# Kernel tuning notes

Hardware: AMD Instinct MI355X
Metric: run time of the kernel (lower is better)

## Reference

```python
import jax, jax.numpy as jnp
import numpy as np

N_NODES = 50000
N_EDGES = 800000
IN_FEATS = 128
OUT_FEATS = 128


def setup_inputs() -> dict:
    key = jax.random.key(0)
    k_feat, k_src, k_dst, k_w1, k_w2, k_lw = jax.random.split(key, 6)
    feat = jax.random.normal(k_feat, (N_NODES, IN_FEATS), dtype=jnp.float32)
    src_idx = jax.random.randint(k_src, (N_EDGES,), 0, N_NODES, dtype=jnp.int64 if jax.config.jax_enable_x64 else jnp.int32)
    dst_idx = jax.random.randint(k_dst, (N_EDGES,), 0, N_NODES, dtype=jnp.int64 if jax.config.jax_enable_x64 else jnp.int32)
    # xavier-uniform-ish scales
    w1_lim = float(np.sqrt(6.0 / (2 * IN_FEATS + IN_FEATS)))
    w2_lim = float(np.sqrt(6.0 / (IN_FEATS + OUT_FEATS)))
    lw_lim = float(np.sqrt(2.0) * np.sqrt(6.0 / (IN_FEATS + OUT_FEATS)))
    weight1 = jax.random.uniform(k_w1, (2 * IN_FEATS, IN_FEATS), jnp.float32, -w1_lim, w1_lim)
    weight2 = jax.random.uniform(k_w2, (IN_FEATS, OUT_FEATS), jnp.float32, -w2_lim, w2_lim)
    loop_weight = jax.random.uniform(k_lw, (IN_FEATS, OUT_FEATS), jnp.float32, -lw_lim, lw_lim)
    bias = jnp.zeros((OUT_FEATS,), dtype=jnp.float32)
    return {
        "feat": feat,
        "src_idx": src_idx,
        "dst_idx": dst_idx,
        "weight1": weight1,
        "weight2": weight2,
        "loop_weight": loop_weight,
        "bias": bias,
    }


def reference(feat, src_idx, dst_idx, weight1, weight2, loop_weight, bias):
    # Gather per-edge src/dst features and concat: [E, 2*d]
    feat_msg = jnp.concatenate([feat[src_idx], feat[dst_idx]], axis=-1)
    # 2-layer edge MLP: relu(msg @ W1) @ W2 -> [E, out]
    e_msg = jnp.matmul(jax.nn.relu(jnp.matmul(feat_msg, weight1)), weight2)
    # Scatter-sum to destination nodes: [N, out]
    rst = jax.ops.segment_sum(e_msg, dst_idx, num_segments=feat.shape[0])
    # bias + residual loop message
    rst = rst + bias + jnp.matmul(feat, loop_weight)
    return rst
```

## Files before the change

### kernel.cpp

```cpp
#include <hip/hip_runtime.h>

typedef __attribute__((ext_vector_type(8))) unsigned short ushort8v;
typedef __attribute__((ext_vector_type(8))) short short8v;
typedef __attribute__((ext_vector_type(4))) float f32x4;

#define CAP 64
#define BINSTRIDE 2560

__device__ inline unsigned short f2bf(float f) {
    union { float f; unsigned u; } v; v.f = f;
    unsigned u = v.u;
    unsigned r = (u + 0x7FFFu + ((u >> 16) & 1u)) >> 16;
    return (unsigned short)r;
}
__device__ inline float bf2f(unsigned short h) {
    union { unsigned u; float f; } v; v.u = ((unsigned)h) << 16;
    return v.f;
}
__device__ inline unsigned pkbf(float lo, float hi) {
    unsigned r;
    asm("v_cvt_pk_bf16_f32 %0, %1, %2" : "=v"(r) : "v"(lo), "v"(hi));
    return r;
}

__global__ __launch_bounds__(256) void prep_weights(
    const float* __restrict__ W1, const float* __restrict__ W2,
    const float* __restrict__ LW,
    unsigned short* __restrict__ W1t, unsigned short* __restrict__ W3t,
    int* __restrict__ binCur, int NBINS) {
    int tid = threadIdx.x;
    if (blockIdx.x == 0)
        for (int j = tid; j < NBINS; j += 256) binCur[j] = 0;
    int i = blockIdx.x * 256 + tid;
    if (i < 32768) {
        int jj = i >> 7, k = i & 127;
        float v = (jj < 128) ? W1[k * 128 + jj] : W1[(128 + k) * 128 + (jj - 128)];
        W1t[i] = f2bf(v);
    } else {
        int i2 = i - 32768;
        int n = i2 >> 8, k = i2 & 255;
        float v = (k < 128) ? W2[k * 128 + n] : LW[(k - 128) * 128 + n];
        W3t[i2] = f2bf(v);
    }
}

__global__ __launch_bounds__(256) void gemm1_bin(
    const float* __restrict__ feat, const unsigned short* __restrict__ W1t,
    unsigned short* __restrict__ AB,
    const int* __restrict__ src, const int* __restrict__ dst,
    int* __restrict__ binCur, unsigned* __restrict__ binPairs,
    int E, int NC, int NT2, int M, int NBINS) {
    __shared__ unsigned short smem[2 * 128 * 64];
    const int tid = threadIdx.x;
    const int bid = blockIdx.x;
    const int r5 = bid % 5;

    if (r5 < 4) {
        int g = (bid / 5) * 4 + r5;
        if (g >= NT2) return;
        int m0 = (g >> 1) * 128, n0 = (g & 1) * 128;
        const int lane = tid & 63, w = tid >> 6;
        const int wr = w >> 1, wc = w & 1;
        const int q = lane >> 4, ln = lane & 15;
        unsigned short* As = smem;
        unsigned short* Bs = smem + 128 * 64;

        f32x4 acc[4][4];
#pragma unroll
        for (int i = 0; i < 4; i++)
#pragma unroll
            for (int j = 0; j < 4; j++) acc[i][j] = (f32x4)0.f;

        for (int kk = 0; kk < 128; kk += 64) {
#pragma unroll
            for (int i = 0; i < 4; i++) {
                int id = i * 256 + tid;
                int r = id >> 3, bb = id & 7, gr = m0 + r;
                unsigned short* dstp = As + r * 64 + ((bb ^ (r & 7)) * 8);
                float4 lo = make_float4(0.f, 0.f, 0.f, 0.f), hi = lo;
                if (gr < M) {
                    const float* p = feat + (size_t)gr * 128 + kk + bb * 8;
                    lo = *(const float4*)p;
                    hi = *(const float4*)(p + 4);
                }
                *(uint4*)dstp = make_uint4(pkbf(lo.x, lo.y), pkbf(lo.z, lo.w),
                                           pkbf(hi.x, hi.y), pkbf(hi.z, hi.w));
            }
#pragma unroll
            for (int i = 0; i < 4; i++) {
                int id = i * 256 + tid;
                int r = id >> 3, bb = id & 7;
                ushort8v v = *(const ushort8v*)(W1t + (size_t)(n0 + r) * 128 + kk + bb * 8);
                *(ushort8v*)(Bs + r * 64 + ((bb ^ (r & 7)) * 8)) = v;
            }
            __syncthreads();
#pragma unroll
            for (int ks = 0; ks < 2; ks++) {
                short8v af[4], bv[4];
#pragma unroll
                for (int ti = 0; ti < 4; ti++) {
                    int m = wr * 64 + ti * 16 + ln;
                    int blk = (ks * 4 + q) ^ (m & 7);
                    af[ti] = *(const short8v*)(As + m * 64 + blk * 8);
                }
#pragma unroll
                for (int tj = 0; tj < 4; tj++) {
                    int n = wc * 64 + tj * 16 + ln;
                    int blk = (ks * 4 + q) ^ (n & 7);
                    bv[tj] = *(const short8v*)(Bs + n * 64 + blk * 8);
                }
#pragma unroll
                for (int ti = 0; ti < 4; ti++)
#pragma unroll
                    for (int tj = 0; tj < 4; tj++)
                        acc[ti][tj] = __builtin_amdgcn_mfma_f32_16x16x32_bf16(
                            af[ti], bv[tj], acc[ti][tj], 0, 0, 0);
            }
            if (kk == 0) __syncthreads();
        }
#pragma unroll
        for (int ti = 0; ti < 4; ti++) {
            int rowb = m0 + wr * 64 + ti * 16 + q * 4;
#pragma unroll
            for (int tj = 0; tj < 4; tj++) {
                int col = n0 + wc * 64 + tj * 16 + ln;
                f32x4 c = acc[ti][tj];
#pragma unroll
                for (int r = 0; r < 4; r++) {
                    int row = rowb + r;
                    if (row < M)
                        AB[(size_t)row * 256 + col] = f2bf(c[r]);
                }
            }
        }
    } else {
        int chunk = bid / 5;
        if (chunk >= NC) return;
        int* hist = (int*)smem;
        int* bse = hist + 512;
        for (int j = tid; j < NBINS; j += 256) hist[j] = 0;

        int s[16], d[16];
        int base = chunk * 4096;
#pragma unroll
        for (int i = 0; i < 4; i++) {
            int e = base + i * 1024 + tid * 4;
            if (e + 3 < E) {
                int4 dv = *(const int4*)(dst + e);
                int4 sv = *(const int4*)(src + e);
                d[i * 4 + 0] = dv.x; d[i * 4 + 1] = dv.y;
                d[i * 4 + 2] = dv.z; d[i * 4 + 3] = dv.w;
                s[i * 4 + 0] = sv.x; s[i * 4 + 1] = sv.y;
                s[i * 4 + 2] = sv.z; s[i * 4 + 3] = sv.w;
            } else {
#pragma unroll
                for (int k = 0; k < 4; k++) {
                    int ee = e + k;
                    if (ee < E) { d[i * 4 + k] = dst[ee]; s[i * 4 + k] = src[ee]; }
                    else d[i * 4 + k] = -1;
                }
            }
        }
        __syncthreads();
#pragma unroll
        for (int k = 0; k < 16; k++)
            if (d[k] >= 0) atomicAdd(&hist[d[k] >> 7], 1);
        __syncthreads();
        for (int j = tid; j < NBINS; j += 256) {
            int c = hist[j];
            bse[j] = c ? atomicAdd(&binCur[j], c) : 0;
            hist[j] = 0;
        }
        __syncthreads();
#pragma unroll
        for (int k = 0; k < 16; k++) {
            if (d[k] < 0) continue;
            int b = d[k] >> 7;
            int p = bse[b] + atomicAdd(&hist[b], 1);
            if (p < BINSTRIDE)
                binPairs[(size_t)b * BINSTRIDE + p] =
                    ((unsigned)(d[k] & 127) << 16) | (unsigned)s[k];
        }
    }
}

__global__ __launch_bounds__(256) void build_buckets(
    const int* __restrict__ binCur, const unsigned* __restrict__ binPairs,
    int* __restrict__ cur, unsigned short* __restrict__ eSrc,
    int N, int NBINS) {
    __shared__ unsigned pairs[BINSTRIDE];
    __shared__ int deg[128], rnk[128];
    int b = blockIdx.x, tid = threadIdx.x;
    if (b >= NBINS) return;
    int cnt = min(binCur[b], BINSTRIDE);
    if (tid < 128) { deg[tid] = 0; rnk[tid] = 0; }
    __syncthreads();
    for (int i = tid; i < cnt; i += 256) {
        unsigned pr = binPairs[(size_t)b * BINSTRIDE + i];
        pairs[i] = pr;
        atomicAdd(&deg[pr >> 16], 1);
    }
    __syncthreads();
    int node0 = b << 7;
    if (tid < 128 && node0 + tid < N) cur[node0 + tid] = deg[tid];
    for (int i = tid; i < cnt; i += 256) {
        unsigned pr = pairs[i];
        int dl = pr >> 16;
        int pos = atomicAdd(&rnk[dl], 1);
        if (pos < CAP)
            eSrc[(size_t)(node0 + dl) * CAP + pos] = (unsigned short)(pr & 0xFFFF);
    }
}

__global__ __launch_bounds__(256) void gather_kernel(
    const unsigned short* __restrict__ AB, const int* __restrict__ cur,
    const unsigned short* __restrict__ eSrc,
    unsigned short* __restrict__ S2, int N) {
    int wid = (blockIdx.x * 256 + threadIdx.x) >> 6;
    int lane = threadIdx.x & 63;
    if (wid >= N) return;
    int num = min(cur[wid], CAP);
    size_t start = (size_t)wid * CAP;
    int half = lane >> 5, ln32 = lane & 31;
    ushort4 bv = *(const ushort4*)(AB + (size_t)wid * 256 + 128 + ln32 * 4);
    float b0 = bf2f(bv.x), b1 = bf2f(bv.y), b2 = bf2f(bv.z), b3 = bf2f(bv.w);
    float p0 = 0.f, p1 = 0.f, p2 = 0.f, p3 = 0.f;

    int mySrc = (lane < num) ? (int)eSrc[start + lane] : 0;
    int j = 0;
    for (; j + 16 <= num; j += 16) {
        ushort4 v[8];
#pragma unroll
        for (int u = 0; u < 8; u++) {
            int s = __shfl(mySrc, j + 2 * u + half);
            v[u] = *(const ushort4*)(AB + (size_t)s * 256 + ln32 * 4);
        }
#pragma unroll
        for (int u = 0; u < 8; u++) {
            p0 += fmaxf(bf2f(v[u].x) + b0, 0.f);
            p1 += fmaxf(bf2f(v[u].y) + b1, 0.f);
            p2 += fmaxf(bf2f(v[u].z) + b2, 0.f);
            p3 += fmaxf(bf2f(v[u].w) + b3, 0.f);
        }
    }
    for (; j + 4 <= num; j += 4) {
        ushort4 v[2];
#pragma unroll
        for (int u = 0; u < 2; u++) {
            int s = __shfl(mySrc, j + 2 * u + half);
            v[u] = *(const ushort4*)(AB + (size_t)s * 256 + ln32 * 4);
        }
#pragma unroll
        for (int u = 0; u < 2; u++) {
            p0 += fmaxf(bf2f(v[u].x) + b0, 0.f);
            p1 += fmaxf(bf2f(v[u].y) + b1, 0.f);
            p2 += fmaxf(bf2f(v[u].z) + b2, 0.f);
            p3 += fmaxf(bf2f(v[u].w) + b3, 0.f);
        }
    }
    for (; j < num; j += 2) {
        int idx = j + half;
        int s = __shfl(mySrc, idx);
        bool ok = idx < num;
        ushort4 v = *(const ushort4*)(AB + (size_t)s * 256 + ln32 * 4);
        float m = ok ? 1.f : 0.f;
        p0 += m * fmaxf(bf2f(v.x) + b0, 0.f);
        p1 += m * fmaxf(bf2f(v.y) + b1, 0.f);
        p2 += m * fmaxf(bf2f(v.z) + b2, 0.f);
        p3 += m * fmaxf(bf2f(v.w) + b3, 0.f);
    }
    p0 += __shfl_xor(p0, 32);
    p1 += __shfl_xor(p1, 32);
    p2 += __shfl_xor(p2, 32);
    p3 += __shfl_xor(p3, 32);
    if (half == 0) {
        *(ushort4*)(S2 + (size_t)wid * 128 + ln32 * 4) =
            make_ushort4(f2bf(p0), f2bf(p1), f2bf(p2), f2bf(p3));
    }
}

__global__ __launch_bounds__(256) void gemm2_kernel(
    const unsigned short* __restrict__ S2, const float* __restrict__ feat,
    const unsigned short* __restrict__ W3t,
    float* __restrict__ out, const float* __restrict__ bias, int M) {
    __shared__ unsigned short smem[2 * 128 * 64];
    unsigned short* As = smem;
    unsigned short* Bs = smem + 128 * 64;
    const int tid = threadIdx.x;
    const int lane = tid & 63, w = tid >> 6;
    const int wr = w >> 1, wc = w & 1;
    const int q = lane >> 4, ln = lane & 15;
    const int m0 = blockIdx.x * 128;

    f32x4 acc[4][4];
#pragma unroll
    for (int i = 0; i < 4; i++)
#pragma unroll
        for (int j = 0; j < 4; j++) acc[i][j] = (f32x4)0.f;

    for (int kk = 0; kk < 256; kk += 64) {
        const bool aF32 = (kk >= 128);
#pragma unroll
        for (int i = 0; i < 4; i++) {
            int id = i * 256 + tid;
            int r = id >> 3, bb = id & 7, gr = m0 + r;
            unsigned short* dstp = As + r * 64 + ((bb ^ (r & 7)) * 8);
            if (aF32) {
                float4 lo = make_float4(0.f, 0.f, 0.f, 0.f), hi = lo;
                if (gr < M) {
                    const float* p = feat + (size_t)gr * 128 + (kk - 128) + bb * 8;
                    lo = *(const float4*)p;
                    hi = *(const float4*)(p + 4);
                }
                *(uint4*)dstp = make_uint4(pkbf(lo.x, lo.y), pkbf(lo.z, lo.w),
                                           pkbf(hi.x, hi.y), pkbf(hi.z, hi.w));
            } else {
                ushort8v v = (ushort8v)(unsigned short)0;
                if (gr < M) v = *(const ushort8v*)(S2 + (size_t)gr * 128 + kk + bb * 8);
                *(ushort8v*)dstp = v;
            }
        }
#pragma unroll
        for (int i = 0; i < 4; i++) {
            int id = i * 256 + tid;
            int r = id >> 3, bb = id & 7;
            ushort8v v = *(const ushort8v*)(W3t + (size_t)r * 256 + kk + bb * 8);
            *(ushort8v*)(Bs + r * 64 + ((bb ^ (r & 7)) * 8)) = v;
        }
        __syncthreads();
#pragma unroll
        for (int ks = 0; ks < 2; ks++) {
            short8v af[4], bv[4];
#pragma unroll
            for (int ti = 0; ti < 4; ti++) {
                int m = wr * 64 + ti * 16 + ln;
                int blk = (ks * 4 + q) ^ (m & 7);
                af[ti] = *(const short8v*)(As + m * 64 + blk * 8);
            }
#pragma unroll
            for (int tj = 0; tj < 4; tj++) {
                int n = wc * 64 + tj * 16 + ln;
                int blk = (ks * 4 + q) ^ (n & 7);
                bv[tj] = *(const short8v*)(Bs + n * 64 + blk * 8);
            }
#pragma unroll
            for (int ti = 0; ti < 4; ti++)
#pragma unroll
                for (int tj = 0; tj < 4; tj++)
                    acc[ti][tj] = __builtin_amdgcn_mfma_f32_16x16x32_bf16(
                        af[ti], bv[tj], acc[ti][tj], 0, 0, 0);
        }
        if (kk + 64 < 256) __syncthreads();
    }

#pragma unroll
    for (int ti = 0; ti < 4; ti++) {
        int rowb = m0 + wr * 64 + ti * 16 + q * 4;
#pragma unroll
        for (int tj = 0; tj < 4; tj++) {
            int col = wc * 64 + tj * 16 + ln;
            f32x4 c = acc[ti][tj];
            float bv = bias[col];
#pragma unroll
            for (int r = 0; r < 4; r++) {
                int row = rowb + r;
                if (row < M)
                    out[(size_t)row * 128 + col] = c[r] + bv;
            }
        }
    }
}

extern "C" void kernel_launch(void* const* d_in, const int* in_sizes, int n_in,
                              void* d_out, int out_size, void* d_ws, size_t ws_size,
                              hipStream_t stream) {
    const float* feat = (const float*)d_in[0];
    const int* src = (const int*)d_in[1];
    const int* dst = (const int*)d_in[2];
    const float* W1 = (const float*)d_in[3];
    const float* W2 = (const float*)d_in[4];
    const float* LW = (const float*)d_in[5];
    const float* bias = (const float*)d_in[6];
    float* out = (float*)d_out;

    const int N = in_sizes[0] / 128;
    const int E = in_sizes[1];
    const int NBINS = (N + 127) / 128;

    char* ws = (char*)d_ws;
    unsigned short* S2 = (unsigned short*)ws;
    size_t off = (size_t)N * 128 * 2;
    unsigned short* AB = (unsigned short*)(ws + off);
    off += (size_t)N * 256 * 2;
    unsigned short* W1t = (unsigned short*)(ws + off);
    off += (size_t)256 * 128 * 2;
    unsigned short* W3t = (unsigned short*)(ws + off);
    off += (size_t)128 * 256 * 2;
    int* cur = (int*)(ws + off);
    off += (size_t)N * 4;
    unsigned short* eSrc = (unsigned short*)(ws + off);
    off += (size_t)N * CAP * 2;
    int* binCur = (int*)(ws + off);
    off += (size_t)NBINS * 4;
    unsigned* binPairs = (unsigned*)(ws + off);
    off += (size_t)NBINS * BINSTRIDE * 4;

    prep_weights<<<256, 256, 0, stream>>>(W1, W2, LW, W1t, W3t, binCur, NBINS);

    int NT2 = ((N + 127) / 128) * 2;
    int NC = (E + 4095) / 4096;
    int NG = (NT2 + 3) / 4;
    int mx = NG > NC ? NG : NC;
    gemm1_bin<<<5 * mx, 256, 0, stream>>>(
        feat, W1t, AB, src, dst, binCur, binPairs, E, NC, NT2, N, NBINS);

    build_buckets<<<NBINS, 256, 0, stream>>>(binCur, binPairs, cur, eSrc, N, NBINS);

    gather_kernel<<<(N + 3) / 4, 256, 0, stream>>>(AB, cur, eSrc, S2, N);

    gemm2_kernel<<<(N + 127) / 128, 256, 0, stream>>>(S2, feat, W3t, out, bias, N);
}
```

Measured before the change: 164.3 us.

## Restructure pipeline: fuse binning with weight prep, loop GEMM with gemm1 and bucket build

Edge binning moves into the weight-prep kernel, and the bin counter is cleared with a memset. The self-loop GEMM (feat @ LoopW + bias) now runs as a third N-tile inside gemm1 and writes out directly. Bucket building runs in the same launch as gemm1, so one kernel launch and one pass over feat in gemm2 go away. The gather kernel now uses 16-byte loads with four edges per iteration. gemm2 shrinks to K=128 and accumulates into out with a read-modify-write, which adds an extra read of out in exchange for fewer launches and less feat traffic.

```diff
diff --git a/kernel.cpp b/kernel.cpp
--- a/kernel.cpp
+++ b/kernel.cpp
@@ -23,47 +23,103 @@
     return r;
 }
 
-__global__ __launch_bounds__(256) void prep_weights(
+__global__ __launch_bounds__(256) void prep_bin(
     const float* __restrict__ W1, const float* __restrict__ W2,
     const float* __restrict__ LW,
-    unsigned short* __restrict__ W1t, unsigned short* __restrict__ W3t,
-    int* __restrict__ binCur, int NBINS) {
-    int tid = threadIdx.x;
-    if (blockIdx.x == 0)
-        for (int j = tid; j < NBINS; j += 256) binCur[j] = 0;
-    int i = blockIdx.x * 256 + tid;
-    if (i < 32768) {
-        int jj = i >> 7, k = i & 127;
-        float v = (jj < 128) ? W1[k * 128 + jj] : W1[(128 + k) * 128 + (jj - 128)];
-        W1t[i] = f2bf(v);
-    } else {
-        int i2 = i - 32768;
-        int n = i2 >> 8, k = i2 & 255;
-        float v = (k < 128) ? W2[k * 128 + n] : LW[(k - 128) * 128 + n];
-        W3t[i2] = f2bf(v);
-    }
-}
-
-__global__ __launch_bounds__(256) void gemm1_bin(
-    const float* __restrict__ feat, const unsigned short* __restrict__ W1t,
-    unsigned short* __restrict__ AB,
+    unsigned short* __restrict__ W1t, unsigned short* __restrict__ W2t,
+    unsigned short* __restrict__ LWt,
     const int* __restrict__ src, const int* __restrict__ dst,
     int* __restrict__ binCur, unsigned* __restrict__ binPairs,
-    int E, int NC, int NT2, int M, int NBINS) {
+    int E, int NCHUNK, int NBINS) {
+    __shared__ int hist[512];
+    __shared__ int bse[512];
+    const int tid = threadIdx.x;
+    const int bid = blockIdx.x;
+
+    if (bid < 256) {
+        int i = bid * 256 + tid;
+        if (i < 32768) {
+            int n = i >> 7, k = i & 127;
+            float v = (n < 128) ? W1[k * 128 + n] : W1[(128 + k) * 128 + (n - 128)];
+            W1t[i] = f2bf(v);
+        } else if (i < 49152) {
+            int i2 = i - 32768;
+            int n = i2 >> 7, k = i2 & 127;
+            W2t[i2] = f2bf(W2[k * 128 + n]);
+        } else {
+            int i3 = i - 49152;
+            int n = i3 >> 7, k = i3 & 127;
+            LWt[i3] = f2bf(LW[k * 128 + n]);
+        }
+        return;
+    }
+    int chunk = bid - 256;
+    if (chunk >= NCHUNK) return;
+    for (int j = tid; j < NBINS; j += 256) hist[j] = 0;
+
+    int s[8], d[8];
+    int base = chunk * 2048 + tid * 8;
+    if (base + 7 < E) {
+        int4 s0 = *(const int4*)(src + base);
+        int4 s1 = *(const int4*)(src + base + 4);
+        int4 d0 = *(const int4*)(dst + base);
+        int4 d1 = *(const int4*)(dst + base + 4);
+        s[0] = s0.x; s[1] = s0.y; s[2] = s0.z; s[3] = s0.w;
+        s[4] = s1.x; s[5] = s1.y; s[6] = s1.z; s[7] = s1.w;
+        d[0] = d0.x; d[1] = d0.y; d[2] = d0.z; d[3] = d0.w;
+        d[4] = d1.x; d[5] = d1.y; d[6] = d1.z; d[7] = d1.w;
+    } else {
+#pragma unroll
+        for (int k = 0; k < 8; k++) {
+            int ee = base + k;
+            if (ee < E) { d[k] = dst[ee]; s[k] = src[ee]; }
+            else d[k] = -1;
+        }
+    }
+    __syncthreads();
+#pragma unroll
+    for (int k = 0; k < 8; k++)
+        if (d[k] >= 0) atomicAdd(&hist[d[k] >> 7], 1);
+    __syncthreads();
+    for (int j = tid; j < NBINS; j += 256) {
+        int c = hist[j];
+        bse[j] = c ? atomicAdd(&binCur[j], c) : 0;
+        hist[j] = 0;
+    }
+    __syncthreads();
+#pragma unroll
+    for (int k = 0; k < 8; k++) {
+        if (d[k] < 0) continue;
+        int b = d[k] >> 7;
+        int p = bse[b] + atomicAdd(&hist[b], 1);
+        if (p < BINSTRIDE)
+            binPairs[(size_t)b * BINSTRIDE + p] =
+                ((unsigned)(d[k] & 127) << 16) | (unsigned)s[k];
+    }
+}
+
+__global__ __launch_bounds__(256) void gemm1_build(
+    const float* __restrict__ feat, const unsigned short* __restrict__ W1t,
+    const unsigned short* __restrict__ LWt, const float* __restrict__ bias,
+    unsigned short* __restrict__ AB, float* __restrict__ out,
+    const int* __restrict__ binCur, const unsigned* __restrict__ binPairs,
+    int* __restrict__ cur, unsigned short* __restrict__ eSrc,
+    int M, int NBINS) {
     __shared__ unsigned short smem[2 * 128 * 64];
     const int tid = threadIdx.x;
     const int bid = blockIdx.x;
-    const int r5 = bid % 5;
-
-    if (r5 < 4) {
-        int g = (bid / 5) * 4 + r5;
-        if (g >= NT2) return;
-        int m0 = (g >> 1) * 128, n0 = (g & 1) * 128;
+    const int r4 = bid & 3;
+
+    if (r4 < 3) {
+        const int m0 = (bid >> 2) * 128;
+        const int nt = r4;
         const int lane = tid & 63, w = tid >> 6;
         const int wr = w >> 1, wc = w & 1;
         const int q = lane >> 4, ln = lane & 15;
         unsigned short* As = smem;
         unsigned short* Bs = smem + 128 * 64;
+        const unsigned short* Bsrc = (nt < 2) ? (W1t + (size_t)(nt * 128) * 128)
+                                              : LWt;
 
         f32x4 acc[4][4];
 #pragma unroll
@@ -90,7 +146,7 @@
             for (int i = 0; i < 4; i++) {
                 int id = i * 256 + tid;
                 int r = id >> 3, bb = id & 7;
-                ushort8v v = *(const ushort8v*)(W1t + (size_t)(n0 + r) * 128 + kk + bb * 8);
+                ushort8v v = *(const ushort8v*)(Bsrc + (size_t)r * 128 + kk + bb * 8);
                 *(ushort8v*)(Bs + r * 64 + ((bb ^ (r & 7)) * 8)) = v;
             }
             __syncthreads();
@@ -123,92 +179,45 @@
             int rowb = m0 + wr * 64 + ti * 16 + q * 4;
 #pragma unroll
             for (int tj = 0; tj < 4; tj++) {
-                int col = n0 + wc * 64 + tj * 16 + ln;
+                int col = wc * 64 + tj * 16 + ln;
                 f32x4 c = acc[ti][tj];
+                float bv2 = (nt == 2) ? bias[col] : 0.f;
 #pragma unroll
                 for (int r = 0; r < 4; r++) {
                     int row = rowb + r;
-                    if (row < M)
-                        AB[(size_t)row * 256 + col] = f2bf(c[r]);
+                    if (row < M) {
+                        if (nt < 2)
+                            AB[(size_t)row * 256 + nt * 128 + col] = f2bf(c[r]);
+                        else
+                            out[(size_t)row * 128 + col] = c[r] + bv2;
+                    }
                 }
             }
         }
     } else {
-        int chunk = bid / 5;
-        if (chunk >= NC) return;
-        int* hist = (int*)smem;
-        int* bse = hist + 512;
-        for (int j = tid; j < NBINS; j += 256) hist[j] = 0;
-
-        int s[16], d[16];
-        int base = chunk * 4096;
-#pragma unroll
-        for (int i = 0; i < 4; i++) {
-            int e = base + i * 1024 + tid * 4;
-            if (e + 3 < E) {
-                int4 dv = *(const int4*)(dst + e);
-                int4 sv = *(const int4*)(src + e);
-                d[i * 4 + 0] = dv.x; d[i * 4 + 1] = dv.y;
-                d[i * 4 + 2] = dv.z; d[i * 4 + 3] = dv.w;
-                s[i * 4 + 0] = sv.x; s[i * 4 + 1] = sv.y;
-                s[i * 4 + 2] = sv.z; s[i * 4 + 3] = sv.w;
-            } else {
-#pragma unroll
-                for (int k = 0; k < 4; k++) {
-                    int ee = e + k;
-                    if (ee < E) { d[i * 4 + k] = dst[ee]; s[i * 4 + k] = src[ee]; }
-                    else d[i * 4 + k] = -1;
-                }
-            }
-        }
+        int b = bid >> 2;
+        if (b >= NBINS) return;
+        unsigned* pairs = (unsigned*)smem;
+        int* deg = (int*)(pairs + BINSTRIDE);
+        int* rnk = deg + 128;
+        int cnt = min(binCur[b], BINSTRIDE);
+        if (tid < 128) { deg[tid] = 0; rnk[tid] = 0; }
         __syncthreads();
-#pragma unroll
-        for (int k = 0; k < 16; k++)
-            if (d[k] >= 0) atomicAdd(&hist[d[k] >> 7], 1);
+        for (int i = tid; i < cnt; i += 256) {
+            unsigned pr = binPairs[(size_t)b * BINSTRIDE + i];
+            pairs[i] = pr;
+            atomicAdd(&deg[pr >> 16], 1);
+        }
         __syncthreads();
-        for (int j = tid; j < NBINS; j += 256) {
-            int c = hist[j];
-            bse[j] = c ? atomicAdd(&binCur[j], c) : 0;
-            hist[j] = 0;
-        }
-        __syncthreads();
-#pragma unroll
-        for (int k = 0; k < 16; k++) {
-            if (d[k] < 0) continue;
-            int b = d[k] >> 7;
-            int p = bse[b] + atomicAdd(&hist[b], 1);
-            if (p < BINSTRIDE)
-                binPairs[(size_t)b * BINSTRIDE + p] =
-                    ((unsigned)(d[k] & 127) << 16) | (unsigned)s[k];
-        }
-    }
-}
-
-__global__ __launch_bounds__(256) void build_buckets(
-    const int* __restrict__ binCur, const unsigned* __restrict__ binPairs,
-    int* __restrict__ cur, unsigned short* __restrict__ eSrc,
-    int N, int NBINS) {
-    __shared__ unsigned pairs[BINSTRIDE];
-    __shared__ int deg[128], rnk[128];
-    int b = blockIdx.x, tid = threadIdx.x;
-    if (b >= NBINS) return;
-    int cnt = min(binCur[b], BINSTRIDE);
-    if (tid < 128) { deg[tid] = 0; rnk[tid] = 0; }
-    __syncthreads();
-    for (int i = tid; i < cnt; i += 256) {
-        unsigned pr = binPairs[(size_t)b * BINSTRIDE + i];
-        pairs[i] = pr;
-        atomicAdd(&deg[pr >> 16], 1);
-    }
-    __syncthreads();
-    int node0 = b << 7;
-    if (tid < 128 && node0 + tid < N) cur[node0 + tid] = deg[tid];
-    for (int i = tid; i < cnt; i += 256) {
-        unsigned pr = pairs[i];
-        int dl = pr >> 16;
-        int pos = atomicAdd(&rnk[dl], 1);
-        if (pos < CAP)
-            eSrc[(size_t)(node0 + dl) * CAP + pos] = (unsigned short)(pr & 0xFFFF);
+        int node0 = b << 7;
+        if (tid < 128 && node0 + tid < M) cur[node0 + tid] = deg[tid];
+        for (int i = tid; i < cnt; i += 256) {
+            unsigned pr = pairs[i];
+            int dl = pr >> 16;
+            int pos = atomicAdd(&rnk[dl], 1);
+            if (pos < CAP)
+                eSrc[(size_t)(node0 + dl) * CAP + pos] = (unsigned short)(pr & 0xFFFF);
+        }
     }
 }
 
@@ -221,68 +230,57 @@
     if (wid >= N) return;
     int num = min(cur[wid], CAP);
     size_t start = (size_t)wid * CAP;
-    int half = lane >> 5, ln32 = lane & 31;
-    ushort4 bv = *(const ushort4*)(AB + (size_t)wid * 256 + 128 + ln32 * 4);
-    float b0 = bf2f(bv.x), b1 = bf2f(bv.y), b2 = bf2f(bv.z), b3 = bf2f(bv.w);
-    float p0 = 0.f, p1 = 0.f, p2 = 0.f, p3 = 0.f;
+    int qw = lane >> 4, lq = lane & 15;
+
+    ushort8v b8 = *(const ushort8v*)(AB + (size_t)wid * 256 + 128 + lq * 8);
+    float b[8], p[8];
+#pragma unroll
+    for (int e = 0; e < 8; e++) { b[e] = bf2f(b8[e]); p[e] = 0.f; }
 
     int mySrc = (lane < num) ? (int)eSrc[start + lane] : 0;
     int j = 0;
     for (; j + 16 <= num; j += 16) {
-        ushort4 v[8];
-#pragma unroll
-        for (int u = 0; u < 8; u++) {
-            int s = __shfl(mySrc, j + 2 * u + half);
-            v[u] = *(const ushort4*)(AB + (size_t)s * 256 + ln32 * 4);
-        }
-#pragma unroll
-        for (int u = 0; u < 8; u++) {
-            p0 += fmaxf(bf2f(v[u].x) + b0, 0.f);
-            p1 += fmaxf(bf2f(v[u].y) + b1, 0.f);
-            p2 += fmaxf(bf2f(v[u].z) + b2, 0.f);
-            p3 += fmaxf(bf2f(v[u].w) + b3, 0.f);
-        }
-    }
-    for (; j + 4 <= num; j += 4) {
-        ushort4 v[2];
-#pragma unroll
-        for (int u = 0; u < 2; u++) {
-            int s = __shfl(mySrc, j + 2 * u + half);
-            v[u] = *(const ushort4*)(AB + (size_t)s * 256 + ln32 * 4);
-        }
-#pragma unroll
-        for (int u = 0; u < 2; u++) {
-            p0 += fmaxf(bf2f(v[u].x) + b0, 0.f);
-            p1 += fmaxf(bf2f(v[u].y) + b1, 0.f);
-            p2 += fmaxf(bf2f(v[u].z) + b2, 0.f);
-            p3 += fmaxf(bf2f(v[u].w) + b3, 0.f);
-        }
-    }
-    for (; j < num; j += 2) {
-        int idx = j + half;
-        int s = __shfl(mySrc, idx);
-        bool ok = idx < num;
-        ushort4 v = *(const ushort4*)(AB + (size_t)s * 256 + ln32 * 4);
-        float m = ok ? 1.f : 0.f;
-        p0 += m * fmaxf(bf2f(v.x) + b0, 0.f);
-        p1 += m * fmaxf(bf2f(v.y) + b1, 0.f);
-        p2 += m * fmaxf(bf2f(v.z) + b2, 0.f);
-        p3 += m * fmaxf(bf2f(v.w) + b3, 0.f);
-    }
-    p0 += __shfl_xor(p0, 32);
-    p1 += __shfl_xor(p1, 32);
-    p2 += __shfl_xor(p2, 32);
-    p3 += __shfl_xor(p3, 32);
-    if (half == 0) {
-        *(ushort4*)(S2 + (size_t)wid * 128 + ln32 * 4) =
-            make_ushort4(f2bf(p0), f2bf(p1), f2bf(p2), f2bf(p3));
+        ushort8v v[4];
+#pragma unroll
+        for (int u = 0; u < 4; u++) {
+            int s = __shfl(mySrc, j + 4 * u + qw);
+            v[u] = *(const ushort8v*)(AB + (size_t)s * 256 + lq * 8);
+        }
+#pragma unroll
+        for (int u = 0; u < 4; u++)
+#pragma unroll
+            for (int e = 0; e < 8; e++)
+                p[e] += fmaxf(bf2f(v[u][e]) + b[e], 0.f);
+    }
+    for (; j < num; j += 4) {
+        int idx = j + qw;
+        int s = __shfl(mySrc, idx & 63);
+        float m = (idx < num) ? 1.f : 0.f;
+        ushort8v v = *(const ushort8v*)(AB + (size_t)s * 256 + lq * 8);
+#pragma unroll
+        for (int e = 0; e < 8; e++)
+            p[e] += m * fmaxf(bf2f(v[e]) + b[e], 0.f);
+    }
+#pragma unroll
+    for (int e = 0; e < 8; e++) {
+        p[e] += __shfl_xor(p[e], 16);
+        p[e] += __shfl_xor(p[e], 32);
+    }
+    if (qw == 0) {
+        ushort8v o;
+#pragma unroll
+        for (int e = 0; e < 8; e += 2) {
+            unsigned pk = pkbf(p[e], p[e + 1]);
+            o[e] = (unsigned short)(pk & 0xFFFF);
+            o[e + 1] = (unsigned short)(pk >> 16);
+        }
+        *(ushort8v*)(S2 + (size_t)wid * 128 + lq * 8) = o;
     }
 }
 
 __global__ __launch_bounds__(256) void gemm2_kernel(
-    const unsigned short* __restrict__ S2, const float* __restrict__ feat,
-    const unsigned short* __restrict__ W3t,
-    float* __restrict__ out, const float* __restrict__ bias, int M) {
+    const unsigned short* __restrict__ S2, const unsigned short* __restrict__ W2t,
+    float* __restrict__ out, int M) {
     __shared__ unsigned short smem[2 * 128 * 64];
     unsigned short* As = smem;
     unsigned short* Bs = smem + 128 * 64;
@@ -298,33 +296,20 @@
 #pragma unroll
         for (int j = 0; j < 4; j++) acc[i][j] = (f32x4)0.f;
 
-    for (int kk = 0; kk < 256; kk += 64) {
-        const bool aF32 = (kk >= 128);
+    for (int kk = 0; kk < 128; kk += 64) {
 #pragma unroll
         for (int i = 0; i < 4; i++) {
             int id = i * 256 + tid;
             int r = id >> 3, bb = id & 7, gr = m0 + r;
-            unsigned short* dstp = As + r * 64 + ((bb ^ (r & 7)) * 8);
-            if (aF32) {
-                float4 lo = make_float4(0.f, 0.f, 0.f, 0.f), hi = lo;
-                if (gr < M) {
-                    const float* p = feat + (size_t)gr * 128 + (kk - 128) + bb * 8;
-                    lo = *(const float4*)p;
-                    hi = *(const float4*)(p + 4);
-                }
-                *(uint4*)dstp = make_uint4(pkbf(lo.x, lo.y), pkbf(lo.z, lo.w),
-                                           pkbf(hi.x, hi.y), pkbf(hi.z, hi.w));
-            } else {
-                ushort8v v = (ushort8v)(unsigned short)0;
-                if (gr < M) v = *(const ushort8v*)(S2 + (size_t)gr * 128 + kk + bb * 8);
-                *(ushort8v*)dstp = v;
-            }
+            ushort8v v = (ushort8v)(unsigned short)0;
+            if (gr < M) v = *(const ushort8v*)(S2 + (size_t)gr * 128 + kk + bb * 8);
+            *(ushort8v*)(As + r * 64 + ((bb ^ (r & 7)) * 8)) = v;
         }
 #pragma unroll
         for (int i = 0; i < 4; i++) {
             int id = i * 256 + tid;
             int r = id >> 3, bb = id & 7;
-            ushort8v v = *(const ushort8v*)(W3t + (size_t)r * 256 + kk + bb * 8);
+            ushort8v v = *(const ushort8v*)(W2t + (size_t)r * 128 + kk + bb * 8);
             *(ushort8v*)(Bs + r * 64 + ((bb ^ (r & 7)) * 8)) = v;
         }
         __syncthreads();
@@ -350,7 +335,7 @@
                     acc[ti][tj] = __builtin_amdgcn_mfma_f32_16x16x32_bf16(
                         af[ti], bv[tj], acc[ti][tj], 0, 0, 0);
         }
-        if (kk + 64 < 256) __syncthreads();
+        if (kk == 0) __syncthreads();
     }
 
 #pragma unroll
@@ -360,12 +345,13 @@
         for (int tj = 0; tj < 4; tj++) {
             int col = wc * 64 + tj * 16 + ln;
             f32x4 c = acc[ti][tj];
-            float bv = bias[col];
 #pragma unroll
             for (int r = 0; r < 4; r++) {
                 int row = rowb + r;
-                if (row < M)
-                    out[(size_t)row * 128 + col] = c[r] + bv;
+                if (row < M) {
+                    size_t o = (size_t)row * 128 + col;
+                    out[o] = out[o] + c[r];
+                }
             }
         }
     }
@@ -394,8 +380,10 @@
     off += (size_t)N * 256 * 2;
     unsigned short* W1t = (unsigned short*)(ws + off);
     off += (size_t)256 * 128 * 2;
-    unsigned short* W3t = (unsigned short*)(ws + off);
-    off += (size_t)128 * 256 * 2;
+    unsigned short* W2t = (unsigned short*)(ws + off);
+    off += (size_t)128 * 128 * 2;
+    unsigned short* LWt = (unsigned short*)(ws + off);
+    off += (size_t)128 * 128 * 2;
     int* cur = (int*)(ws + off);
     off += (size_t)N * 4;
     unsigned short* eSrc = (unsigned short*)(ws + off);
@@ -405,18 +393,16 @@
     unsigned* binPairs = (unsigned*)(ws + off);
     off += (size_t)NBINS * BINSTRIDE * 4;
 
-    prep_weights<<<256, 256, 0, stream>>>(W1, W2, LW, W1t, W3t, binCur, NBINS);
-
-    int NT2 = ((N + 127) / 128) * 2;
-    int NC = (E + 4095) / 4096;
-    int NG = (NT2 + 3) / 4;
-    int mx = NG > NC ? NG : NC;
-    gemm1_bin<<<5 * mx, 256, 0, stream>>>(
-        feat, W1t, AB, src, dst, binCur, binPairs, E, NC, NT2, N, NBINS);
-
-    build_buckets<<<NBINS, 256, 0, stream>>>(binCur, binPairs, cur, eSrc, N, NBINS);
+    const int NCHUNK = (E + 2047) / 2048;
+
+    hipMemsetAsync(binCur, 0, (size_t)NBINS * 4, stream);
+    prep_bin<<<256 + NCHUNK, 256, 0, stream>>>(
+        W1, W2, LW, W1t, W2t, LWt, src, dst, binCur, binPairs, E, NCHUNK, NBINS);
+
+    gemm1_build<<<4 * NBINS, 256, 0, stream>>>(
+        feat, W1t, LWt, bias, AB, out, binCur, binPairs, cur, eSrc, N, NBINS);
 
     gather_kernel<<<(N + 3) / 4, 256, 0, stream>>>(AB, cur, eSrc, S2, N);
 
-    gemm2_kernel<<<(N + 127) / 128, 256, 0, stream>>>(S2, feat, W3t, out, bias, N);
-}
+    gemm2_kernel<<<NBINS, 256, 0, stream>>>(S2, W2t, out, N);
+}
```

Result: slower. 199.5 us (+21.4%).
